# Optimization experiments

Hardware: AMD Instinct MI355X
Metric: run time of the kernel (lower is better)

Reference implementation:

```python
import jax, jax.numpy as jnp
import numpy as np
import math

WS = 8      # window_size
SS = 4      # stride = window_size // 2
NHEADS = 4

def _grid(size, ws, ss):
    n = (size - ws) // ss + 1
    return jnp.arange(n)[:, None] * ss + jnp.arange(ws)[None, :]  # (n, ws)

def _unfold(x, ws, ss):
    # x: (B,C,Hp,Wp) -> (B, L, C, ws*ws), matching torch F.unfold ordering
    B, C, Hp, Wp = x.shape
    ri = _grid(Hp, ws, ss)
    ci = _grid(Wp, ws, ss)
    p = x[:, :, ri][:, :, :, :, ci]  # (B,C,nH,ws,nW,ws)
    nH, nW = ri.shape[0], ci.shape[0]
    p = p.transpose(0, 2, 4, 1, 3, 5).reshape(B, nH * nW, C, ws * ws)
    return p, nH, nW

def _fold(p, Hp, Wp, nH, nW, ws, ss):
    # p: (B, L, C, ws*ws) -> overlap-add to (B,C,Hp,Wp), matching torch F.fold
    B, L, C, _ = p.shape
    p = p.reshape(B, nH, nW, C, ws, ws).transpose(0, 3, 1, 4, 2, 5)  # (B,C,nH,ws,nW,ws)
    rr = _grid(Hp, ws, ss)[:, :, None, None]   # (nH,ws,1,1)
    cc = _grid(Wp, ws, ss)[None, None, :, :]   # (1,1,nW,ws)
    return jnp.zeros((B, C, Hp, Wp), p.dtype).at[:, :, rr, cc].add(p)

def _se(h, w1, w2):
    # squeeze-excite: global avg pool -> 1x1 reduce -> relu -> 1x1 expand -> sigmoid gate
    pooled = h.mean(axis=(2, 3))                                # (B, gc)
    s = jax.nn.sigmoid(jax.nn.relu(pooled @ w1.T) @ w2.T)       # (B, gc)
    return h * s[:, :, None, None]

def _forward(low, high, w_ql, w_kh, w_vh, w_qh, w_kl, w_vl, w_proj_l, w_proj_h,
             se0_w1, se0_w2, se1_w1, se1_w2, se2_w1, se2_w2):
    B, C, H, W = low.shape
    ws, ss = WS, SS
    n_h = 0 if H <= ws else math.ceil((H - ws) / ss)
    n_w = 0 if W <= ws else math.ceil((W - ws) / ss)
    Hp, Wp = n_h * ss + ws, n_w * ss + ws
    pad = ((0, 0), (0, 0), (0, Hp - H), (0, Wp - W))
    low_p = jnp.pad(low, pad)
    high_p = jnp.pad(high, pad)
    base, rem = divmod(C, 3)
    chs = [base + (1 if i < rem else 0) for i in range(3)]
    ofs = np.cumsum([0] + chs)
    sew = [(se0_w1, se0_w2), (se1_w1, se1_w2), (se2_w1, se2_w2)]
    high_dir = jnp.concatenate(
        [_se(high_p[:, ofs[i]:ofs[i + 1]], *sew[i]) for i in range(3)], axis=1)
    lw, nH, nW = _unfold(low_p, ws, ss)    # (B,L,C,Np)
    hw, _, _ = _unfold(high_dir, ws, ss)
    L, Np, d = lw.shape[1], ws * ws, C // NHEADS
    scale = d ** -0.5
    proj = lambda x, w: jnp.einsum('oc,blcn->blon', w, x).reshape(B, L, NHEADS, d, Np)
    a_lh = jax.nn.softmax(jnp.einsum('blhdn,blhdm->blhnm', proj(lw, w_ql), proj(hw, w_kh)) * scale, axis=-1)
    a_hl = jax.nn.softmax(jnp.einsum('blhdn,blhdm->blhnm', proj(hw, w_qh), proj(lw, w_kl)) * scale, axis=-1)
    ol = jnp.einsum('blhnm,blhdm->blhdn', a_lh, proj(hw, w_vh)).reshape(B, L, C, Np)
    oh = jnp.einsum('blhnm,blhdm->blhdn', a_hl, proj(lw, w_vl)).reshape(B, L, C, Np)
    mask = _fold(jnp.ones((1, L, 1, Np), low.dtype), Hp, Wp, nH, nW, ws, ss)  # overlap counts
    out_l = (_fold(ol, Hp, Wp, nH, nW, ws, ss) / mask)[:, :, :H, :W]
    out_h = (_fold(oh, Hp, Wp, nH, nW, ws, ss) / mask)[:, :, :H, :W]
    return (low + jnp.einsum('oc,bchw->bohw', w_proj_l, out_l),
            high + jnp.einsum('oc,bchw->bohw', w_proj_h, out_h))

def setup_inputs() -> dict:
    key = jax.random.key(0)
    ks = jax.random.split(key, 20)
    B, C, H, W = 4, 64, 128, 128
    chs = [22, 21, 21]
    d = {
        'low': jax.random.normal(ks[0], (B, C, H, W), jnp.float32),
        'high': jax.random.normal(ks[1], (B, C, H, W), jnp.float32),
    }
    for i, n in enumerate(['w_ql', 'w_kh', 'w_vh', 'w_qh', 'w_kl', 'w_vl', 'w_proj_l', 'w_proj_h']):
        d[n] = jax.random.normal(ks[2 + i], (C, C), jnp.float32) * (C ** -0.5)
    for i, gc in enumerate(chs):
        d[f'se{i}_w1'] = jax.random.normal(ks[10 + 2 * i], (1, gc), jnp.float32) * 0.1
        d[f'se{i}_w2'] = jax.random.normal(ks[11 + 2 * i], (gc, 1), jnp.float32) * 0.1
    return d

def reference(low, high, w_ql, w_kh, w_vh, w_qh, w_kl, w_vl, w_proj_l, w_proj_h,
              se0_w1, se0_w2, se1_w1, se1_w2, se2_w1, se2_w2):
    return _forward(low, high, w_ql, w_kh, w_vh, w_qh, w_kl, w_vl, w_proj_l, w_proj_h,
                    se0_w1, se0_w2, se1_w1, se1_w2, se2_w1, se2_w2)
```

## Files before the change

kernel.cpp:

```cpp
#include <hip/hip_runtime.h>

typedef short short8 __attribute__((ext_vector_type(8)));
typedef short short4v __attribute__((ext_vector_type(4)));
typedef float f4 __attribute__((ext_vector_type(4)));

#define NB 4
#define NHW 128
#define NPX (NHW*NHW)
#define NWIN 31
#define NL (NWIN*NWIN)
#define SWV(r,c) (((r)<<6) + (((((c)>>3) ^ ((r)&7))<<3) | ((c)&7)))
#define MFMA(a,b,c) __builtin_amdgcn_mfma_f32_16x16x32_bf16(a,b,c,0,0,0)

__device__ __forceinline__ short f2bf(float f) {
    unsigned u = __float_as_uint(f);
    u += 0x7fffu + ((u >> 16) & 1u);
    return (short)(u >> 16);
}
__device__ __forceinline__ float bf2f(short v) {
    return __uint_as_float(((unsigned)(unsigned short)v) << 16);
}

__global__ void k_pool(const float* __restrict__ high, float* __restrict__ pooled) {
    int bc = blockIdx.x;
    const float* src = high + (size_t)bc * NPX;
    float s = 0.f;
    for (int i = threadIdx.x; i < NPX; i += 256) s += src[i];
    for (int off = 32; off > 0; off >>= 1) s += __shfl_down(s, off);
    __shared__ float red[4];
    int lane = threadIdx.x & 63, wv = threadIdx.x >> 6;
    if (lane == 0) red[wv] = s;
    __syncthreads();
    if (threadIdx.x == 0)
        pooled[bc] = (red[0] + red[1] + red[2] + red[3]) * (1.f / NPX);
}

__global__ void k_gate(const float* __restrict__ pooled,
                       const float* __restrict__ w10, const float* __restrict__ w20,
                       const float* __restrict__ w11, const float* __restrict__ w21,
                       const float* __restrict__ w12, const float* __restrict__ w22,
                       float* __restrict__ sgate) {
    __shared__ float pl[256];
    int t = threadIdx.x;
    pl[t] = pooled[t];
    __syncthreads();
    int b = t >> 6, c = t & 63;
    const float* w1; const float* w2; int o0, gc;
    if (c < 22)      { w1 = w10; w2 = w20; o0 = 0;  gc = 22; }
    else if (c < 43) { w1 = w11; w2 = w21; o0 = 22; gc = 21; }
    else             { w1 = w12; w2 = w22; o0 = 43; gc = 21; }
    float a = 0.f;
    for (int k = 0; k < gc; ++k) a += pl[b*64 + o0 + k] * w1[k];
    a = fmaxf(a, 0.f);
    float z = a * w2[c - o0];
    sgate[t] = 1.f / (1.f + __expf(-z));
}

__device__ __forceinline__ void wrange(int x, int& lo, int& hi) {
    lo = (x >= 7) ? ((x - 4) >> 2) : 0;
    hi = x >> 2; if (hi > 30) hi = 30;
}

template<int EMIT>
__global__ __launch_bounds__(256, 4) void k_proj(
    const float* __restrict__ src, const float* __restrict__ gate,
    const float* __restrict__ Wq, const float* __restrict__ Wk, const float* __restrict__ Wv,
    short* __restrict__ Qp, short* __restrict__ Kp, short* __restrict__ Vp) {
    __shared__ float T[64*129];
    int b = blockIdx.x >> 7, row = blockIdx.x & 127;
    int t = threadIdx.x;
    const float* sp = src + (size_t)b*64*NPX + row*NHW;
    #pragma unroll
    for (int i = 0; i < 8; ++i) {
        int f = t + i*256;
        int c = f >> 5, p4 = (f & 31) << 2;
        float4 v = *(const float4*)(sp + (size_t)c*NPX + p4);
        float g = gate ? gate[b*64 + c] : 1.f;
        T[c*129 + p4 + 0] = v.x * g;
        T[c*129 + p4 + 1] = v.y * g;
        T[c*129 + p4 + 2] = v.z * g;
        T[c*129 + p4 + 3] = v.w * g;
    }
    __syncthreads();
    int w = t >> 6, ln = t & 63, l16 = ln & 15, quad = ln >> 4;
    int orow = 16*w + l16;
    short8 wq[2], wk[2], wv[2];
    #pragma unroll
    for (int kf = 0; kf < 2; ++kf) {
        if (EMIT & 1) {
            const float* p = Wq + orow*64 + kf*32 + quad*8;
            #pragma unroll
            for (int j = 0; j < 8; ++j) wq[kf][j] = f2bf(p[j]);
        }
        if (EMIT & 2) {
            const float* p = Wk + orow*64 + kf*32 + quad*8;
            #pragma unroll
            for (int j = 0; j < 8; ++j) wk[kf][j] = f2bf(p[j]);
        }
        if (EMIT & 4) {
            const float* p = Wv + orow*64 + kf*32 + quad*8;
            #pragma unroll
            for (int j = 0; j < 8; ++j) wv[kf][j] = f2bf(p[j]);
        }
    }
    #pragma unroll
    for (int nt = 0; nt < 8; ++nt) {
        int px = nt*16 + l16;
        short8 xb[2];
        #pragma unroll
        for (int kf = 0; kf < 2; ++kf) {
            const float* p = T + (kf*32 + quad*8)*129 + px;
            #pragma unroll
            for (int j = 0; j < 8; ++j) xb[kf][j] = f2bf(p[j*129]);
        }
        size_t clbase = ((size_t)b*NPX + row*NHW + px)*64 + 16*w + quad*4;
        if (EMIT & 1) {
            f4 acc = {0.f,0.f,0.f,0.f};
            acc = MFMA(wq[0], xb[0], acc); acc = MFMA(wq[1], xb[1], acc);
            short4v sv;
            #pragma unroll
            for (int r = 0; r < 4; ++r) sv[r] = f2bf(acc[r]);
            *(short4v*)(Qp + clbase) = sv;
        }
        if (EMIT & 2) {
            f4 acc = {0.f,0.f,0.f,0.f};
            acc = MFMA(wk[0], xb[0], acc); acc = MFMA(wk[1], xb[1], acc);
            short4v sv;
            #pragma unroll
            for (int r = 0; r < 4; ++r) sv[r] = f2bf(acc[r]);
            *(short4v*)(Kp + clbase) = sv;
        }
        if (EMIT & 4) {
            f4 acc = {0.f,0.f,0.f,0.f};
            acc = MFMA(wv[0], xb[0], acc); acc = MFMA(wv[1], xb[1], acc);
            #pragma unroll
            for (int r = 0; r < 4; ++r)
                Vp[((size_t)(b*64 + 16*w + quad*4 + r))*NPX + row*NHW + px] = f2bf(acc[r]);
        }
    }
}

__global__ __launch_bounds__(256, 4) void k_attn(
    const short* __restrict__ Qp, const short* __restrict__ Kp,
    const short* __restrict__ Vp, short* __restrict__ scr, int nb) {
    __shared__ __align__(16) short Pb[4][1024];
    int bidx = blockIdx.x;
    int b = bidx / NL, l = bidx - b*NL;
    int wr = l / NWIN, wc = l - (l/NWIN)*NWIN;
    int row0 = wr*4, col0 = wc*4;
    int parity = (wr & 1)*2 + (wc & 1);
    int t = threadIdx.x, w = t >> 6, ln = t & 63, l16 = ln & 15, quad = ln >> 4;
    int h = w;
    short* PT = Pb[w];
    short8 z = {0,0,0,0,0,0,0,0};

    short8 kb[4];
    #pragma unroll
    for (int mt = 0; mt < 4; ++mt) {
        int m = mt*16 + l16;
        int px = (row0 + (m >> 3))*NHW + col0 + (m & 7);
        kb[mt] = (quad < 2) ? *(const short8*)(Kp + ((size_t)b*NPX + px)*64 + h*16 + quad*8) : z;
    }
    short8 va0, va1;
    {
        const short* vb = Vp + ((size_t)(b*64 + h*16 + l16))*NPX;
        const short* p0 = vb + (row0 + quad)*NHW + col0;
        const short* p1 = vb + (row0 + 4 + quad)*NHW + col0;
        short4v a = *(const short4v*)p0, bq = *(const short4v*)(p0 + 4);
        short4v c = *(const short4v*)p1, d = *(const short4v*)(p1 + 4);
        #pragma unroll
        for (int j = 0; j < 4; ++j) { va0[j] = a[j]; va0[4+j] = bq[j]; va1[j] = c[j]; va1[4+j] = d[j]; }
    }

    #pragma unroll
    for (int ntl = 0; ntl < 4; ++ntl) {
        int n = ntl*16 + l16;
        int px = (row0 + (n >> 3))*NHW + col0 + (n & 7);
        short8 qa = (quad < 2) ? *(const short8*)(Qp + ((size_t)b*NPX + px)*64 + h*16 + quad*8) : z;
        f4 s[4];
        #pragma unroll
        for (int mt = 0; mt < 4; ++mt) {
            f4 acc = {0.f,0.f,0.f,0.f};
            s[mt] = MFMA(qa, kb[mt], acc);
        }
        f4 sum = {0.f,0.f,0.f,0.f};
        #pragma unroll
        for (int mt = 0; mt < 4; ++mt)
            #pragma unroll
            for (int r = 0; r < 4; ++r) {
                float e = __expf(fminf(s[mt][r]*0.25f, 30.f));
                s[mt][r] = e; sum[r] += e;
            }
        #pragma unroll
        for (int d = 1; d < 16; d <<= 1)
            #pragma unroll
            for (int r = 0; r < 4; ++r) sum[r] += __shfl_xor(sum[r], d);
        #pragma unroll
        for (int r = 0; r < 4; ++r) sum[r] = 1.f / sum[r];
        #pragma unroll
        for (int mt = 0; mt < 4; ++mt)
            #pragma unroll
            for (int r = 0; r < 4; ++r)
                PT[SWV(quad*4 + r, mt*16 + l16)] = f2bf(s[mt][r] * sum[r]);
        f4 o = {0.f,0.f,0.f,0.f};
        o = MFMA(va0, *(const short8*)(PT + SWV(l16, quad*8)), o);
        o = MFMA(va1, *(const short8*)(PT + SWV(l16, 32 + quad*8)), o);
        short4v sv;
        #pragma unroll
        for (int r = 0; r < 4; ++r) sv[r] = f2bf(o[r]);
        *(short4v*)(scr + (((size_t)(parity*nb + b))*NPX + px)*64 + h*16 + quad*4) = sv;
    }
}

__global__ __launch_bounds__(256, 4) void k_gather(
    const short* __restrict__ scr, const float* __restrict__ resid,
    const float* __restrict__ wproj, float* __restrict__ outp, int nb) {
    __shared__ __align__(16) short G[8192];
    int bidx = blockIdx.x, b = bidx >> 7, hh = bidx & 127;
    int t = threadIdx.x;
    int p = t >> 1, c0 = (t & 1)*32;
    int rlo, rhi, clo, chi;
    wrange(hh, rlo, rhi); wrange(p, clo, chi);
    float vr[2], vc[2];
    vr[0] = (rhi > rlo || (rlo & 1) == 0) ? 1.f : 0.f;
    vr[1] = (rhi > rlo || (rlo & 1) == 1) ? 1.f : 0.f;
    vc[0] = (chi > clo || (clo & 1) == 0) ? 1.f : 0.f;
    vc[1] = (chi > clo || (clo & 1) == 1) ? 1.f : 0.f;
    float g[32];
    #pragma unroll
    for (int k = 0; k < 32; ++k) g[k] = 0.f;
    #pragma unroll
    for (int par = 0; par < 4; ++par) {
        float wgt = vr[par >> 1] * vc[par & 1];
        const short* srcp = scr + (((size_t)(par*nb + b))*NPX + hh*NHW + p)*64 + c0;
        #pragma unroll
        for (int k4 = 0; k4 < 4; ++k4) {
            short8 v = *(const short8*)(srcp + k4*8);
            #pragma unroll
            for (int j = 0; j < 8; ++j) g[k4*8 + j] += wgt * bf2f(v[j]);
        }
    }
    float inv = 1.f / ((float)(rhi - rlo + 1) * (float)(chi - clo + 1));
    #pragma unroll
    for (int k4 = 0; k4 < 4; ++k4) {
        short8 v;
        #pragma unroll
        for (int j = 0; j < 8; ++j) v[j] = f2bf(g[k4*8 + j] * inv);
        *(short8*)(G + SWV(p, c0 + k4*8)) = v;
    }
    __syncthreads();
    int w = t >> 6, ln = t & 63, l16 = ln & 15, quad = ln >> 4;
    short8 wa0, wa1;
    {
        const float* p0 = wproj + (16*w + l16)*64 + quad*8;
        #pragma unroll
        for (int j = 0; j < 8; ++j) { wa0[j] = f2bf(p0[j]); wa1[j] = f2bf(p0[32 + j]); }
    }
    #pragma unroll
    for (int pt = 0; pt < 8; ++pt) {
        f4 acc = {0.f,0.f,0.f,0.f};
        acc = MFMA(wa0, *(const short8*)(G + SWV(pt*16 + l16, quad*8)), acc);
        acc = MFMA(wa1, *(const short8*)(G + SWV(pt*16 + l16, 32 + quad*8)), acc);
        #pragma unroll
        for (int r = 0; r < 4; ++r) {
            size_t gi = (((size_t)(b*64 + 16*w + quad*4 + r))*NHW + hh)*NHW + pt*16 + l16;
            outp[gi] = resid[gi] + acc[r];
        }
    }
}

extern "C" void kernel_launch(void* const* d_in, const int* in_sizes, int n_in,
                              void* d_out, int out_size, void* d_ws, size_t ws_size,
                              hipStream_t stream) {
    const float* low  = (const float*)d_in[0];
    const float* high = (const float*)d_in[1];
    const float* w_ql = (const float*)d_in[2];
    const float* w_kh = (const float*)d_in[3];
    const float* w_vh = (const float*)d_in[4];
    const float* w_qh = (const float*)d_in[5];
    const float* w_kl = (const float*)d_in[6];
    const float* w_vl = (const float*)d_in[7];
    const float* w_pl = (const float*)d_in[8];
    const float* w_ph = (const float*)d_in[9];
    float* out = (float*)d_out;
    float* pooled = (float*)d_ws;
    float* sgate  = pooled + 256;
    short* base = (short*)((char*)d_ws + 2048);
    const size_t PL = (size_t)NB * NPX * 64;
    const size_t plane_f = (size_t)NB * 64 * NPX;
    size_t need_full = 2048 + (6*PL + 4*PL) * sizeof(short);
    size_t scr_elems_per_b = 4 * (size_t)NPX * 64;

    k_pool<<<dim3(NB*64), dim3(256), 0, stream>>>(high, pooled);
    k_gate<<<dim3(1), dim3(256), 0, stream>>>(pooled,
        (const float*)d_in[10], (const float*)d_in[11],
        (const float*)d_in[12], (const float*)d_in[13],
        (const float*)d_in[14], (const float*)d_in[15], sgate);

    if (ws_size >= need_full) {
        short* QL = base;        short* KL = base + PL;   short* VL = base + 2*PL;
        short* QH = base + 3*PL; short* KH = base + 4*PL; short* VH = base + 5*PL;
        short* scr = base + 6*PL;
        k_proj<7><<<dim3(NB*NHW), dim3(256), 0, stream>>>(low,  nullptr, w_ql, w_kl, w_vl, QL, KL, VL);
        k_proj<7><<<dim3(NB*NHW), dim3(256), 0, stream>>>(high, sgate,   w_qh, w_kh, w_vh, QH, KH, VH);
        k_attn<<<dim3(NB*NL), dim3(256), 0, stream>>>(QL, KH, VH, scr, NB);
        k_gather<<<dim3(NB*NHW), dim3(256), 0, stream>>>(scr, low, w_pl, out, NB);
        k_attn<<<dim3(NB*NL), dim3(256), 0, stream>>>(QH, KL, VL, scr, NB);
        k_gather<<<dim3(NB*NHW), dim3(256), 0, stream>>>(scr, high, w_ph, out + plane_f, NB);
    } else {
        short* P0 = base; short* P1 = base + PL; short* P2 = base + 2*PL;
        short* scr = base + 3*PL;
        int nbc = 0;
        for (int n = NB; n >= 1; n >>= 1)
            if (ws_size >= 2048 + (3*PL + n*scr_elems_per_b)*sizeof(short)) { nbc = n; break; }
        if (nbc == 0) nbc = 1;
        for (int pass = 0; pass < 2; ++pass) {
            const float* qsrc = pass ? high : low;
            const float* ksrc = pass ? low  : high;
            const float* qg   = pass ? sgate : nullptr;
            const float* kg   = pass ? nullptr : sgate;
            const float* Wq   = pass ? w_qh : w_ql;
            const float* Wk   = pass ? w_kl : w_kh;
            const float* Wv   = pass ? w_vl : w_vh;
            const float* Wp   = pass ? w_ph : w_pl;
            const float* resid = pass ? high : low;
            float* op = out + (size_t)pass * plane_f;
            k_proj<1><<<dim3(NB*NHW), dim3(256), 0, stream>>>(qsrc, qg, Wq, nullptr, nullptr, P0, nullptr, nullptr);
            k_proj<6><<<dim3(NB*NHW), dim3(256), 0, stream>>>(ksrc, kg, nullptr, Wk, Wv, nullptr, P1, P2);
            for (int b0 = 0; b0 < NB; b0 += nbc) {
                int nb = (NB - b0) < nbc ? (NB - b0) : nbc;
                size_t boff = (size_t)b0 * NPX * 64;
                k_attn<<<dim3(nb*NL), dim3(256), 0, stream>>>(P0 + boff, P1 + boff, P2 + boff, scr, nb);
                k_gather<<<dim3(nb*NHW), dim3(256), 0, stream>>>(scr, resid + boff, Wp, op + boff, nb);
            }
        }
    }
}
```

Baseline: 247.6 us.

## Batch both attention directions per launch and stage bf16 swizzled tile in k_proj

The two cross-attention directions (low→high and high→low) now share one k_attn launch and one k_gather launch with a doubled grid, provided the workspace can hold two scratch buffers. This removes two launches and the tail gaps between them. k_proj now converts inputs to bf16 while staging them into a swizzled 16 KB LDS tile, so the MFMA operand becomes a single vector load in place of 16 scalar fp32 loads and converts. It also shrinks LDS so more blocks fit, and the launch-bounds occupancy hints are raised, which may add register pressure.

Measured after the change: 317.7 us. 1.28x slower.

```diff
diff --git a/kernel.cpp b/kernel.cpp
--- a/kernel.cpp
+++ b/kernel.cpp
@@ -62,24 +62,24 @@
 }
 
 template<int EMIT>
-__global__ __launch_bounds__(256, 4) void k_proj(
+__global__ __launch_bounds__(256, 6) void k_proj(
     const float* __restrict__ src, const float* __restrict__ gate,
     const float* __restrict__ Wq, const float* __restrict__ Wk, const float* __restrict__ Wv,
     short* __restrict__ Qp, short* __restrict__ Kp, short* __restrict__ Vp) {
-    __shared__ float T[64*129];
+    __shared__ __align__(16) short T[8192];
     int b = blockIdx.x >> 7, row = blockIdx.x & 127;
     int t = threadIdx.x;
     const float* sp = src + (size_t)b*64*NPX + row*NHW;
     #pragma unroll
     for (int i = 0; i < 8; ++i) {
         int f = t + i*256;
-        int c = f >> 5, p4 = (f & 31) << 2;
-        float4 v = *(const float4*)(sp + (size_t)c*NPX + p4);
+        int c = f & 63, px = (f >> 6) << 2;
+        float4 v = *(const float4*)(sp + (size_t)c*NPX + px);
         float g = gate ? gate[b*64 + c] : 1.f;
-        T[c*129 + p4 + 0] = v.x * g;
-        T[c*129 + p4 + 1] = v.y * g;
-        T[c*129 + p4 + 2] = v.z * g;
-        T[c*129 + p4 + 3] = v.w * g;
+        T[SWV(px + 0, c)] = f2bf(v.x * g);
+        T[SWV(px + 1, c)] = f2bf(v.y * g);
+        T[SWV(px + 2, c)] = f2bf(v.z * g);
+        T[SWV(px + 3, c)] = f2bf(v.w * g);
     }
     __syncthreads();
     int w = t >> 6, ln = t & 63, l16 = ln & 15, quad = ln >> 4;
@@ -106,17 +106,12 @@
     #pragma unroll
     for (int nt = 0; nt < 8; ++nt) {
         int px = nt*16 + l16;
-        short8 xb[2];
-        #pragma unroll
-        for (int kf = 0; kf < 2; ++kf) {
-            const float* p = T + (kf*32 + quad*8)*129 + px;
-            #pragma unroll
-            for (int j = 0; j < 8; ++j) xb[kf][j] = f2bf(p[j*129]);
-        }
+        short8 xb0 = *(const short8*)(T + SWV(px, quad*8));
+        short8 xb1 = *(const short8*)(T + SWV(px, 32 + quad*8));
         size_t clbase = ((size_t)b*NPX + row*NHW + px)*64 + 16*w + quad*4;
         if (EMIT & 1) {
             f4 acc = {0.f,0.f,0.f,0.f};
-            acc = MFMA(wq[0], xb[0], acc); acc = MFMA(wq[1], xb[1], acc);
+            acc = MFMA(wq[0], xb0, acc); acc = MFMA(wq[1], xb1, acc);
             short4v sv;
             #pragma unroll
             for (int r = 0; r < 4; ++r) sv[r] = f2bf(acc[r]);
@@ -124,7 +119,7 @@
         }
         if (EMIT & 2) {
             f4 acc = {0.f,0.f,0.f,0.f};
-            acc = MFMA(wk[0], xb[0], acc); acc = MFMA(wk[1], xb[1], acc);
+            acc = MFMA(wk[0], xb0, acc); acc = MFMA(wk[1], xb1, acc);
             short4v sv;
             #pragma unroll
             for (int r = 0; r < 4; ++r) sv[r] = f2bf(acc[r]);
@@ -132,7 +127,7 @@
         }
         if (EMIT & 4) {
             f4 acc = {0.f,0.f,0.f,0.f};
-            acc = MFMA(wv[0], xb[0], acc); acc = MFMA(wv[1], xb[1], acc);
+            acc = MFMA(wv[0], xb0, acc); acc = MFMA(wv[1], xb1, acc);
             #pragma unroll
             for (int r = 0; r < 4; ++r)
                 Vp[((size_t)(b*64 + 16*w + quad*4 + r))*NPX + row*NHW + px] = f2bf(acc[r]);
@@ -140,12 +135,19 @@
     }
 }
 
-__global__ __launch_bounds__(256, 4) void k_attn(
-    const short* __restrict__ Qp, const short* __restrict__ Kp,
-    const short* __restrict__ Vp, short* __restrict__ scr, int nb) {
+__global__ __launch_bounds__(256, 8) void k_attn(
+    const short* __restrict__ Q0, const short* __restrict__ K0, const short* __restrict__ V0,
+    const short* __restrict__ Q1, const short* __restrict__ K1, const short* __restrict__ V1,
+    short* __restrict__ scr, size_t scr_stride, int nb) {
     __shared__ __align__(16) short Pb[4][1024];
     int bidx = blockIdx.x;
-    int b = bidx / NL, l = bidx - b*NL;
+    int per = nb * NL;
+    int pass = bidx / per; int rem2 = bidx - pass*per;
+    int b = rem2 / NL, l = rem2 - b*NL;
+    const short* Qp = pass ? Q1 : Q0;
+    const short* Kp = pass ? K1 : K0;
+    const short* Vp = pass ? V1 : V0;
+    short* scrp = scr + (size_t)pass * scr_stride;
     int wr = l / NWIN, wc = l - (l/NWIN)*NWIN;
     int row0 = wr*4, col0 = wc*4;
     int parity = (wr & 1)*2 + (wc & 1);
@@ -208,15 +210,24 @@
         short4v sv;
         #pragma unroll
         for (int r = 0; r < 4; ++r) sv[r] = f2bf(o[r]);
-        *(short4v*)(scr + (((size_t)(parity*nb + b))*NPX + px)*64 + h*16 + quad*4) = sv;
-    }
-}
-
-__global__ __launch_bounds__(256, 4) void k_gather(
-    const short* __restrict__ scr, const float* __restrict__ resid,
-    const float* __restrict__ wproj, float* __restrict__ outp, int nb) {
+        *(short4v*)(scrp + (((size_t)(parity*nb + b))*NPX + px)*64 + h*16 + quad*4) = sv;
+    }
+}
+
+__global__ __launch_bounds__(256, 6) void k_gather(
+    const short* __restrict__ scr, size_t scr_stride,
+    const float* __restrict__ r0, const float* __restrict__ r1,
+    const float* __restrict__ wp0, const float* __restrict__ wp1,
+    float* __restrict__ o0, float* __restrict__ o1, int nb) {
     __shared__ __align__(16) short G[8192];
-    int bidx = blockIdx.x, b = bidx >> 7, hh = bidx & 127;
+    int bidx = blockIdx.x;
+    int per = nb * NHW;
+    int pass = bidx / per; int rem2 = bidx - pass*per;
+    int b = rem2 >> 7, hh = rem2 & 127;
+    const short* scrp = scr + (size_t)pass * scr_stride;
+    const float* resid = pass ? r1 : r0;
+    const float* wproj = pass ? wp1 : wp0;
+    float* outp = pass ? o1 : o0;
     int t = threadIdx.x;
     int p = t >> 1, c0 = (t & 1)*32;
     int rlo, rhi, clo, chi;
@@ -232,7 +243,7 @@
     #pragma unroll
     for (int par = 0; par < 4; ++par) {
         float wgt = vr[par >> 1] * vc[par & 1];
-        const short* srcp = scr + (((size_t)(par*nb + b))*NPX + hh*NHW + p)*64 + c0;
+        const short* srcp = scrp + (((size_t)(par*nb + b))*NPX + hh*NHW + p)*64 + c0;
         #pragma unroll
         for (int k4 = 0; k4 < 4; ++k4) {
             short8 v = *(const short8*)(srcp + k4*8);
@@ -288,7 +299,9 @@
     short* base = (short*)((char*)d_ws + 2048);
     const size_t PL = (size_t)NB * NPX * 64;
     const size_t plane_f = (size_t)NB * 64 * NPX;
-    size_t need_full = 2048 + (6*PL + 4*PL) * sizeof(short);
+    const size_t SCR = 4 * PL;
+    size_t need_fused  = 2048 + (6*PL + 2*SCR) * sizeof(short);
+    size_t need_serial = 2048 + (6*PL + SCR) * sizeof(short);
     size_t scr_elems_per_b = 4 * (size_t)NPX * 64;
 
     k_pool<<<dim3(NB*64), dim3(256), 0, stream>>>(high, pooled);
@@ -297,16 +310,24 @@
         (const float*)d_in[12], (const float*)d_in[13],
         (const float*)d_in[14], (const float*)d_in[15], sgate);
 
-    if (ws_size >= need_full) {
+    if (ws_size >= need_serial) {
         short* QL = base;        short* KL = base + PL;   short* VL = base + 2*PL;
         short* QH = base + 3*PL; short* KH = base + 4*PL; short* VH = base + 5*PL;
         short* scr = base + 6*PL;
         k_proj<7><<<dim3(NB*NHW), dim3(256), 0, stream>>>(low,  nullptr, w_ql, w_kl, w_vl, QL, KL, VL);
         k_proj<7><<<dim3(NB*NHW), dim3(256), 0, stream>>>(high, sgate,   w_qh, w_kh, w_vh, QH, KH, VH);
-        k_attn<<<dim3(NB*NL), dim3(256), 0, stream>>>(QL, KH, VH, scr, NB);
-        k_gather<<<dim3(NB*NHW), dim3(256), 0, stream>>>(scr, low, w_pl, out, NB);
-        k_attn<<<dim3(NB*NL), dim3(256), 0, stream>>>(QH, KL, VL, scr, NB);
-        k_gather<<<dim3(NB*NHW), dim3(256), 0, stream>>>(scr, high, w_ph, out + plane_f, NB);
+        if (ws_size >= need_fused) {
+            k_attn<<<dim3(2*NB*NL), dim3(256), 0, stream>>>(QL, KH, VH, QH, KL, VL, scr, SCR, NB);
+            k_gather<<<dim3(2*NB*NHW), dim3(256), 0, stream>>>(scr, SCR, low, high,
+                w_pl, w_ph, out, out + plane_f, NB);
+        } else {
+            k_attn<<<dim3(NB*NL), dim3(256), 0, stream>>>(QL, KH, VH, nullptr, nullptr, nullptr, scr, 0, NB);
+            k_gather<<<dim3(NB*NHW), dim3(256), 0, stream>>>(scr, 0, low, nullptr,
+                w_pl, nullptr, out, nullptr, NB);
+            k_attn<<<dim3(NB*NL), dim3(256), 0, stream>>>(QH, KL, VL, nullptr, nullptr, nullptr, scr, 0, NB);
+            k_gather<<<dim3(NB*NHW), dim3(256), 0, stream>>>(scr, 0, high, nullptr,
+                w_ph, nullptr, out + plane_f, nullptr, NB);
+        }
     } else {
         short* P0 = base; short* P1 = base + PL; short* P2 = base + 2*PL;
         short* scr = base + 3*PL;
@@ -330,8 +351,10 @@
             for (int b0 = 0; b0 < NB; b0 += nbc) {
                 int nb = (NB - b0) < nbc ? (NB - b0) : nbc;
                 size_t boff = (size_t)b0 * NPX * 64;
-                k_attn<<<dim3(nb*NL), dim3(256), 0, stream>>>(P0 + boff, P1 + boff, P2 + boff, scr, nb);
-                k_gather<<<dim3(nb*NHW), dim3(256), 0, stream>>>(scr, resid + boff, Wp, op + boff, nb);
+                k_attn<<<dim3(nb*NL), dim3(256), 0, stream>>>(P0 + boff, P1 + boff, P2 + boff,
+                    nullptr, nullptr, nullptr, scr, 0, nb);
+                k_gather<<<dim3(nb*NHW), dim3(256), 0, stream>>>(scr, 0, resid + boff, nullptr,
+                    Wp, nullptr, op + boff, nullptr, nb);
             }
         }
     }
```
